# Kernel tuning notes

Measured on AMD Instinct MI355X. Metric: run time of the kernel, lower is better.

Reference implementation:

```python
import jax, jax.numpy as jnp
import numpy as np

B, N, C, DP, H, P = 1, 768, 384, 128, 12, 4
HP3 = H * P * 3


def setup_inputs() -> dict:
    key = jax.random.key(0)
    ks = jax.random.split(key, 16)
    w = lambda k, shp: (jax.random.normal(k, shp, jnp.float32) * 0.02)
    inp = {
        'single': jax.random.normal(ks[0], (B, N, C), jnp.float32),
        'pair': jax.random.normal(ks[1], (B, N, N, DP), jnp.float32),
        'rot': jax.random.normal(ks[2], (B, N, 3, 3), jnp.float32),
        'trans': jax.random.normal(ks[3], (B, N, 3), jnp.float32),
        'q_w': w(ks[4], (C, C)), 'q_b': jnp.zeros((C,), jnp.float32),
        'k_w': w(ks[5], (C, C)), 'k_b': jnp.zeros((C,), jnp.float32),
        'v_w': w(ks[6], (C, C)), 'v_b': jnp.zeros((C,), jnp.float32),
        'pb_w': w(ks[7], (H, DP)), 'pb_b': jnp.zeros((H,), jnp.float32),
        'qp_w': w(ks[8], (HP3, C)), 'qp_b': jnp.zeros((HP3,), jnp.float32),
        'kp_w': w(ks[9], (HP3, C)), 'kp_b': jnp.zeros((HP3,), jnp.float32),
        'vp_w': w(ks[10], (HP3, C)), 'vp_b': jnp.zeros((HP3,), jnp.float32),
        'pt_w': w(ks[11], (C, HP3)), 'pt_b': jnp.zeros((C,), jnp.float32),
        'out_w': w(ks[12], (C, C)), 'out_b': jnp.zeros((C,), jnp.float32),
        'ln_g': jnp.ones((C,), jnp.float32), 'ln_b': jnp.zeros((C,), jnp.float32),
    }
    return inp


def _lin(x, w, b):
    return x @ w.T + b


def reference(single, pair, rot, trans, q_w, q_b, k_w, k_b, v_w, v_b,
              pb_w, pb_b, qp_w, qp_b, kp_w, kp_b, vp_w, vp_b,
              pt_w, pt_b, out_w, out_b, ln_g, ln_b):
    Bs, Ns, Cs = single.shape
    Ch = Cs // H
    scale = Ch ** (-0.5)

    q = _lin(single, q_w, q_b).reshape(Bs, Ns, H, Ch)
    k = _lin(single, k_w, k_b).reshape(Bs, Ns, H, Ch)
    v = _lin(single, v_w, v_b).reshape(Bs, Ns, H, Ch)

    pair_bias = jnp.transpose(_lin(pair, pb_w, pb_b), (0, 3, 1, 2))  # b h i j

    def to_global(w_, b_):
        pts = _lin(single, w_, b_).reshape(Bs, Ns, H, P, 3)
        return jnp.einsum('bnhpi,bnij->bnhpj', pts, rot) + trans[:, :, None, None, :]

    qg = to_global(qp_w, qp_b)
    kg = to_global(kp_w, kp_b)

    q2 = jnp.sum(qg * qg, axis=(3, 4))  # b n h
    k2 = jnp.sum(kg * kg, axis=(3, 4))
    qk = jnp.einsum('bihpd,bjhpd->bijh', qg, kg)
    point_logits = -0.5 * (q2[:, :, None, :] + k2[:, None, :, :] - 2.0 * qk)  # b i j h
    point_logits = jnp.transpose(point_logits, (0, 3, 1, 2)) * scale  # b h i j

    scalar_logits = jnp.einsum('bnhc,bmhc->bhnm', q, k) * scale
    attn = jax.nn.softmax(scalar_logits + pair_bias + point_logits, axis=-1)

    weighted = jnp.einsum('bhnm,bmhc->bnhc', attn, v).reshape(Bs, Ns, Cs)

    vg = to_global(vp_w, vp_b)
    point_weighted = jnp.einsum('bhnm,bmhpd->bnhpd', attn, vg).reshape(Bs, Ns, HP3)
    point_proj = _lin(point_weighted, pt_w, pt_b)

    out = _lin(weighted + point_proj, out_w, out_b)
    x = single + out
    mu = jnp.mean(x, axis=-1, keepdims=True)
    var = jnp.var(x, axis=-1, keepdims=True)
    return (x - mu) / jnp.sqrt(var + 1e-5) * ln_g + ln_b
```

## Files before the change

kernel.cpp:

```cpp
#include <hip/hip_runtime.h>
#include <hip/hip_bf16.h>
#include <cstddef>

#define NN 768
#define CC 384
#define HH 12
#define DPP 128
#define OFF_Q   0
#define OFF_K   294912
#define OFF_V   589824
#define OFF_QP  884736
#define OFF_KP  995328
#define OFF_VP  1105920
#define OFF_WTD 1216512
#define OFF_PW  1511424
#define OFF_LOG 1622016

__global__ __launch_bounds__(256) void k_proj(
    const float* __restrict__ single,
    const float* __restrict__ qw, const float* __restrict__ qb,
    const float* __restrict__ kw, const float* __restrict__ kb,
    const float* __restrict__ vw, const float* __restrict__ vb,
    const float* __restrict__ qpw, const float* __restrict__ qpb,
    const float* __restrict__ kpw, const float* __restrict__ kpb,
    const float* __restrict__ vpw, const float* __restrict__ vpb,
    float* __restrict__ ws)
{
    __shared__ float As[64][33];
    __shared__ float Bs[48][33];
    const int tid = threadIdx.x;
    const int i0 = blockIdx.y * 64;
    const int n0 = blockIdx.x * 48;
    const int tx = tid & 15, ty = tid >> 4;
    float acc[4][3] = {};
    for (int k0 = 0; k0 < CC; k0 += 32) {
        #pragma unroll
        for (int l = tid; l < 64 * 32; l += 256) {
            int r = l >> 5, c = l & 31;
            As[r][c] = single[(size_t)(i0 + r) * CC + k0 + c];
        }
        #pragma unroll
        for (int l = tid; l < 48 * 32; l += 256) {
            int r = l >> 5, c = l & 31;
            int n = n0 + r;
            const float* wp; int row;
            if (n < 1152) { int m = n / CC; row = n - m * CC; wp = (m == 0) ? qw : ((m == 1) ? kw : vw); }
            else { int np = n - 1152; int m = np / 144; row = np - m * 144; wp = (m == 0) ? qpw : ((m == 1) ? kpw : vpw); }
            Bs[r][c] = wp[(size_t)row * CC + k0 + c];
        }
        __syncthreads();
        #pragma unroll
        for (int kk = 0; kk < 32; ++kk) {
            float av[4], bv[3];
            #pragma unroll
            for (int a = 0; a < 4; ++a) av[a] = As[ty * 4 + a][kk];
            #pragma unroll
            for (int b = 0; b < 3; ++b) bv[b] = Bs[tx * 3 + b][kk];
            #pragma unroll
            for (int a = 0; a < 4; ++a)
                #pragma unroll
                for (int b = 0; b < 3; ++b)
                    acc[a][b] = fmaf(av[a], bv[b], acc[a][b]);
        }
        __syncthreads();
    }
    #pragma unroll
    for (int a = 0; a < 4; ++a) {
        int i = i0 + ty * 4 + a;
        #pragma unroll
        for (int b = 0; b < 3; ++b) {
            int n = n0 + tx * 3 + b;
            float bias; size_t dst;
            if (n < 1152) {
                int m = n / CC; int c = n - m * CC;
                bias = ((m == 0) ? qb : ((m == 1) ? kb : vb))[c];
                dst = (size_t)m * 294912 + (size_t)i * CC + c;
            } else {
                int np = n - 1152; int m = np / 144; int c = np - m * 144;
                bias = ((m == 0) ? qpb : ((m == 1) ? kpb : vpb))[c];
                dst = (size_t)OFF_QP + (size_t)m * 110592 + (size_t)i * 144 + c;
            }
            ws[dst] = acc[a][b] + bias;
        }
    }
}

__global__ __launch_bounds__(256) void k_to_global(
    const float* __restrict__ rot, const float* __restrict__ trans, float* __restrict__ ws)
{
    int id = blockIdx.x * 256 + threadIdx.x;
    if (id >= 3 * NN * 48) return;
    int t3 = id / (NN * 48);
    int rem = id - t3 * (NN * 48);
    int n = rem / 48;
    int hp = rem - n * 48;
    float* arr = ws + OFF_QP + (size_t)t3 * 110592 + (size_t)n * 144 + hp * 3;
    float p0 = arr[0], p1 = arr[1], p2 = arr[2];
    const float* R = rot + (size_t)n * 9;
    const float* T = trans + (size_t)n * 3;
    arr[0] = p0 * R[0] + p1 * R[3] + p2 * R[6] + T[0];
    arr[1] = p0 * R[1] + p1 * R[4] + p2 * R[7] + T[1];
    arr[2] = p0 * R[2] + p1 * R[5] + p2 * R[8] + T[2];
}

__global__ __launch_bounds__(256) void k_logits(
    const float* __restrict__ pair,
    const float* __restrict__ pbw, const float* __restrict__ pbb,
    const float* __restrict__ q, const float* __restrict__ k,
    const float* __restrict__ qg, const float* __restrict__ kg,
    float* __restrict__ logits)
{
    const float scale = 0.17677669529663687f;
    __shared__ float pbw_s[HH * DPP];
    const int tid = threadIdx.x;
    for (int idx = tid; idx < HH * DPP; idx += 256) pbw_s[idx] = pbw[idx];
    __syncthreads();
    const int i0 = blockIdx.x * 4;
    const int j = blockIdx.y * 256 + tid;

    float acc[4][12];
    #pragma unroll
    for (int ii = 0; ii < 4; ++ii)
        #pragma unroll
        for (int h = 0; h < HH; ++h) acc[ii][h] = pbb[h];

    #pragma unroll
    for (int ii = 0; ii < 4; ++ii) {
        const float4* pr = (const float4*)(pair + ((size_t)(i0 + ii) * NN + j) * DPP);
        #pragma unroll 4
        for (int k4 = 0; k4 < 32; ++k4) {
            float4 pv = pr[k4];
            #pragma unroll
            for (int h = 0; h < HH; ++h) {
                float4 w = ((const float4*)pbw_s)[h * 32 + k4];
                acc[ii][h] = fmaf(pv.x, w.x, acc[ii][h]);
                acc[ii][h] = fmaf(pv.y, w.y, acc[ii][h]);
                acc[ii][h] = fmaf(pv.z, w.z, acc[ii][h]);
                acc[ii][h] = fmaf(pv.w, w.w, acc[ii][h]);
            }
        }
    }

    #pragma unroll
    for (int h = 0; h < HH; ++h) {
        float kf[32];
        const float4* kp4 = (const float4*)(k + (size_t)j * CC + h * 32);
        #pragma unroll
        for (int t = 0; t < 8; ++t) {
            float4 tv = kp4[t];
            kf[4 * t + 0] = tv.x; kf[4 * t + 1] = tv.y; kf[4 * t + 2] = tv.z; kf[4 * t + 3] = tv.w;
        }
        float kgf[12];
        const float4* kg4 = (const float4*)(kg + (size_t)j * 144 + h * 12);
        #pragma unroll
        for (int t = 0; t < 3; ++t) {
            float4 tv = kg4[t];
            kgf[4 * t + 0] = tv.x; kgf[4 * t + 1] = tv.y; kgf[4 * t + 2] = tv.z; kgf[4 * t + 3] = tv.w;
        }
        #pragma unroll
        for (int ii = 0; ii < 4; ++ii) {
            const float* qrow = q + (size_t)(i0 + ii) * CC + h * 32;
            float dt = 0.f;
            #pragma unroll
            for (int c = 0; c < 32; ++c) dt = fmaf(kf[c], qrow[c], dt);
            const float* qgrow = qg + (size_t)(i0 + ii) * 144 + h * 12;
            float pt = 0.f;
            #pragma unroll
            for (int e = 0; e < 12; ++e) { float d2 = qgrow[e] - kgf[e]; pt = fmaf(d2, d2, pt); }
            float lv = acc[ii][h] + scale * dt - 0.5f * scale * pt;
            logits[((size_t)h * NN + (i0 + ii)) * NN + j] = lv;
        }
    }
}

__global__ __launch_bounds__(256) void k_soft(
    const float* __restrict__ logits, const float* __restrict__ v, const float* __restrict__ vg,
    float* __restrict__ weighted, float* __restrict__ pw)
{
    __shared__ float att[8][772];
    __shared__ float vt[128][45];
    const int tid = threadIdx.x;
    const int h = blockIdx.y;
    const int i0 = blockIdx.x * 8;

    for (int idx = tid; idx < 8 * 192; idx += 256) {
        int r = idx / 192, c4 = idx - r * 192;
        float4 tv = ((const float4*)(logits + ((size_t)h * NN + i0 + r) * NN))[c4];
        float* dp = &att[r][c4 * 4];
        dp[0] = tv.x; dp[1] = tv.y; dp[2] = tv.z; dp[3] = tv.w;
    }
    __syncthreads();
    {
        int r = tid >> 5, lane = tid & 31;
        float m = -1e30f;
        for (int jj = lane; jj < NN; jj += 32) m = fmaxf(m, att[r][jj]);
        #pragma unroll
        for (int off = 16; off; off >>= 1) m = fmaxf(m, __shfl_xor(m, off, 32));
        float s = 0.f;
        for (int jj = lane; jj < NN; jj += 32) { float e = __expf(att[r][jj] - m); att[r][jj] = e; s += e; }
        #pragma unroll
        for (int off = 16; off; off >>= 1) s += __shfl_xor(s, off, 32);
        float inv = 1.f / s;
        for (int jj = lane; jj < NN; jj += 32) att[r][jj] *= inv;
    }
    __syncthreads();

    float acc0 = 0.f, acc1 = 0.f;
    const int o0 = tid, o1 = tid + 256;
    const int r0 = o0 / 44, d0 = o0 - r0 * 44;
    const int o1c = (o1 < 352) ? o1 : 351;
    const int r1 = o1c / 44, d1 = o1c - r1 * 44;
    for (int jc = 0; jc < 6; ++jc) {
        for (int idx = tid; idx < 128 * 44; idx += 256) {
            int jj = idx / 44, d = idx - jj * 44;
            int jg = jc * 128 + jj;
            vt[jj][d] = (d < 32) ? v[(size_t)jg * CC + h * 32 + d]
                                 : vg[(size_t)jg * 144 + h * 12 + (d - 32)];
        }
        __syncthreads();
        const float* a0p = &att[r0][jc * 128];
        const float* a1p = &att[r1][jc * 128];
        #pragma unroll 4
        for (int jj = 0; jj < 128; ++jj) {
            acc0 = fmaf(a0p[jj], vt[jj][d0], acc0);
            acc1 = fmaf(a1p[jj], vt[jj][d1], acc1);
        }
        __syncthreads();
    }
    {
        int i = i0 + r0;
        if (d0 < 32) weighted[(size_t)i * CC + h * 32 + d0] = acc0;
        else         pw[(size_t)i * 144 + h * 12 + (d0 - 32)] = acc0;
    }
    if (o1 < 352) {
        int i = i0 + r1;
        if (d1 < 32) weighted[(size_t)i * CC + h * 32 + d1] = acc1;
        else         pw[(size_t)i * 144 + h * 12 + (d1 - 32)] = acc1;
    }
}

__global__ __launch_bounds__(384) void k_out(
    const float* __restrict__ single,
    const float* __restrict__ weighted, const float* __restrict__ pwv,
    const float* __restrict__ ptw, const float* __restrict__ ptb,
    const float* __restrict__ outw, const float* __restrict__ outb,
    const float* __restrict__ lng, const float* __restrict__ lnb,
    float* __restrict__ out)
{
    __shared__ float pw_s[4][144];
    __shared__ float tmp_s[4][388];
    __shared__ float red[16];
    const int tid = threadIdx.x;
    const int i0 = blockIdx.x * 4;
    for (int idx = tid; idx < 4 * 144; idx += 384) {
        int r = idx / 144, e = idx - r * 144;
        pw_s[r][e] = pwv[(size_t)(i0 + r) * 144 + e];
    }
    __syncthreads();
    const int c = tid;
    float t[4];
    {
        float a[4] = {0.f, 0.f, 0.f, 0.f};
        const float4* wp4 = (const float4*)(ptw + (size_t)c * 144);
        #pragma unroll 4
        for (int e4 = 0; e4 < 36; ++e4) {
            float4 w4 = wp4[e4];
            #pragma unroll
            for (int r = 0; r < 4; ++r) {
                float4 pv = *(const float4*)&pw_s[r][e4 * 4];
                a[r] = fmaf(w4.x, pv.x, a[r]);
                a[r] = fmaf(w4.y, pv.y, a[r]);
                a[r] = fmaf(w4.z, pv.z, a[r]);
                a[r] = fmaf(w4.w, pv.w, a[r]);
            }
        }
        float pb = ptb[c];
        #pragma unroll
        for (int r = 0; r < 4; ++r)
            t[r] = weighted[(size_t)(i0 + r) * CC + c] + pb + a[r];
    }
    #pragma unroll
    for (int r = 0; r < 4; ++r) tmp_s[r][c] = t[r];
    __syncthreads();
    float o[4];
    {
        float ob = outb[c];
        #pragma unroll
        for (int r = 0; r < 4; ++r) o[r] = ob;
        const float4* wp4 = (const float4*)(outw + (size_t)c * CC);
        #pragma unroll 2
        for (int e4 = 0; e4 < 96; ++e4) {
            float4 w4 = wp4[e4];
            #pragma unroll
            for (int r = 0; r < 4; ++r) {
                float4 tv = *(const float4*)&tmp_s[r][e4 * 4];
                o[r] = fmaf(w4.x, tv.x, o[r]);
                o[r] = fmaf(w4.y, tv.y, o[r]);
                o[r] = fmaf(w4.z, tv.z, o[r]);
                o[r] = fmaf(w4.w, tv.w, o[r]);
            }
        }
        #pragma unroll
        for (int r = 0; r < 4; ++r) o[r] += single[(size_t)(i0 + r) * CC + c];
    }
    float g = lng[c], bb = lnb[c];
    #pragma unroll
    for (int rr = 0; rr < 4; ++rr) {
        float xs = o[rr], xq = o[rr] * o[rr];
        #pragma unroll
        for (int off = 32; off; off >>= 1) {
            xs += __shfl_xor(xs, off, 64);
            xq += __shfl_xor(xq, off, 64);
        }
        __syncthreads();
        if ((tid & 63) == 0) { int w = tid >> 6; red[w] = xs; red[8 + w] = xq; }
        __syncthreads();
        float S = red[0] + red[1] + red[2] + red[3] + red[4] + red[5];
        float Q = red[8] + red[9] + red[10] + red[11] + red[12] + red[13];
        float mu = S * (1.f / 384.f);
        float var = Q * (1.f / 384.f) - mu * mu;
        float rs = rsqrtf(var + 1e-5f);
        out[(size_t)(i0 + rr) * CC + c] = (o[rr] - mu) * rs * g + bb;
    }
}

extern "C" void kernel_launch(void* const* d_in, const int* in_sizes, int n_in,
                              void* d_out, int out_size, void* d_ws, size_t ws_size,
                              hipStream_t stream)
{
    const float* single = (const float*)d_in[0];
    const float* pair   = (const float*)d_in[1];
    const float* rot    = (const float*)d_in[2];
    const float* trans  = (const float*)d_in[3];
    const float* qw  = (const float*)d_in[4];  const float* qb  = (const float*)d_in[5];
    const float* kw  = (const float*)d_in[6];  const float* kb  = (const float*)d_in[7];
    const float* vw  = (const float*)d_in[8];  const float* vb  = (const float*)d_in[9];
    const float* pbw = (const float*)d_in[10]; const float* pbb = (const float*)d_in[11];
    const float* qpw = (const float*)d_in[12]; const float* qpb = (const float*)d_in[13];
    const float* kpw = (const float*)d_in[14]; const float* kpb = (const float*)d_in[15];
    const float* vpw = (const float*)d_in[16]; const float* vpb = (const float*)d_in[17];
    const float* ptw = (const float*)d_in[18]; const float* ptb = (const float*)d_in[19];
    const float* outw = (const float*)d_in[20]; const float* outb = (const float*)d_in[21];
    const float* lng  = (const float*)d_in[22]; const float* lnb  = (const float*)d_in[23];

    float* ws = (float*)d_ws;
    float* q   = ws + OFF_Q;
    float* k   = ws + OFF_K;
    float* v   = ws + OFF_V;
    float* qg  = ws + OFF_QP;
    float* kg  = ws + OFF_KP;
    float* vg  = ws + OFF_VP;
    float* wtd = ws + OFF_WTD;
    float* pwv = ws + OFF_PW;
    float* logits = ws + OFF_LOG;

    dim3 g1(33, 12);
    hipLaunchKernelGGL(k_proj, g1, dim3(256), 0, stream,
                       single, qw, qb, kw, kb, vw, vb, qpw, qpb, kpw, kpb, vpw, vpb, ws);
    hipLaunchKernelGGL(k_to_global, dim3(432), dim3(256), 0, stream, rot, trans, ws);
    dim3 g3(192, 3);
    hipLaunchKernelGGL(k_logits, g3, dim3(256), 0, stream,
                       pair, pbw, pbb, q, k, qg, kg, logits);
    dim3 g4(96, 12);
    hipLaunchKernelGGL(k_soft, g4, dim3(256), 0, stream, logits, v, vg, wtd, pwv);
    hipLaunchKernelGGL(k_out, dim3(192), dim3(384), 0, stream,
                       single, wtd, pwv, ptw, ptb, outw, outb, lng, lnb, (float*)d_out);
}
```

Before: 320.7 us.

## Transpose V/VG storage, read directly in softmax-AV, halve logits rows per block

The projection kernel now writes V and the value points transposed (feature-major, sequence contiguous), and a new kernel rotates those points in that layout. The softmax kernel drops its shared-memory staging of V and has 176 threads stream float4 rows of V straight from global memory against the attention rows. The logits kernel now handles 2 query rows per block instead of 4 (twice as many blocks) and reads pair-bias weights directly from global memory instead of shared memory. The goal is fewer syncs and shared-memory traffic plus more parallelism, at the cost of idle threads in the softmax kernel and more global or cached weight reads.

```diff
diff --git a/kernel.cpp b/kernel.cpp
--- a/kernel.cpp
+++ b/kernel.cpp
@@ -74,11 +74,13 @@
             if (n < 1152) {
                 int m = n / CC; int c = n - m * CC;
                 bias = ((m == 0) ? qb : ((m == 1) ? kb : vb))[c];
-                dst = (size_t)m * 294912 + (size_t)i * CC + c;
+                if (m == 2) dst = (size_t)OFF_V + (size_t)c * NN + i;
+                else        dst = (size_t)m * 294912 + (size_t)i * CC + c;
             } else {
                 int np = n - 1152; int m = np / 144; int c = np - m * 144;
                 bias = ((m == 0) ? qpb : ((m == 1) ? kpb : vpb))[c];
-                dst = (size_t)OFF_QP + (size_t)m * 110592 + (size_t)i * 144 + c;
+                if (m == 2) dst = (size_t)OFF_VP + (size_t)c * NN + i;
+                else        dst = (size_t)OFF_QP + (size_t)m * 110592 + (size_t)i * 144 + c;
             }
             ws[dst] = acc[a][b] + bias;
         }
@@ -89,7 +91,7 @@
     const float* __restrict__ rot, const float* __restrict__ trans, float* __restrict__ ws)
 {
     int id = blockIdx.x * 256 + threadIdx.x;
-    if (id >= 3 * NN * 48) return;
+    if (id >= 2 * NN * 48) return;
     int t3 = id / (NN * 48);
     int rem = id - t3 * (NN * 48);
     int n = rem / 48;
@@ -103,6 +105,24 @@
     arr[2] = p0 * R[2] + p1 * R[5] + p2 * R[8] + T[2];
 }
 
+__global__ __launch_bounds__(256) void k_to_global_v(
+    const float* __restrict__ rot, const float* __restrict__ trans, float* __restrict__ ws)
+{
+    int id = blockIdx.x * 256 + threadIdx.x;
+    if (id >= 48 * NN) return;
+    int hp = id / NN;
+    int n = id - hp * NN;
+    float* r0 = ws + OFF_VP + (size_t)(hp * 3 + 0) * NN + n;
+    float* r1 = ws + OFF_VP + (size_t)(hp * 3 + 1) * NN + n;
+    float* r2 = ws + OFF_VP + (size_t)(hp * 3 + 2) * NN + n;
+    float p0 = *r0, p1 = *r1, p2 = *r2;
+    const float* R = rot + (size_t)n * 9;
+    const float* T = trans + (size_t)n * 3;
+    *r0 = p0 * R[0] + p1 * R[3] + p2 * R[6] + T[0];
+    *r1 = p0 * R[1] + p1 * R[4] + p2 * R[7] + T[1];
+    *r2 = p0 * R[2] + p1 * R[5] + p2 * R[8] + T[2];
+}
+
 __global__ __launch_bounds__(256) void k_logits(
     const float* __restrict__ pair,
     const float* __restrict__ pbw, const float* __restrict__ pbb,
@@ -111,33 +131,35 @@
     float* __restrict__ logits)
 {
     const float scale = 0.17677669529663687f;
-    __shared__ float pbw_s[HH * DPP];
     const int tid = threadIdx.x;
-    for (int idx = tid; idx < HH * DPP; idx += 256) pbw_s[idx] = pbw[idx];
-    __syncthreads();
-    const int i0 = blockIdx.x * 4;
+    const int i0 = blockIdx.x * 2;
     const int j = blockIdx.y * 256 + tid;
 
-    float acc[4][12];
-    #pragma unroll
-    for (int ii = 0; ii < 4; ++ii)
+    float acc[2][12];
+    #pragma unroll
+    for (int ii = 0; ii < 2; ++ii)
         #pragma unroll
         for (int h = 0; h < HH; ++h) acc[ii][h] = pbb[h];
 
-    #pragma unroll
-    for (int ii = 0; ii < 4; ++ii) {
-        const float4* pr = (const float4*)(pair + ((size_t)(i0 + ii) * NN + j) * DPP);
-        #pragma unroll 4
-        for (int k4 = 0; k4 < 32; ++k4) {
-            float4 pv = pr[k4];
-            #pragma unroll
-            for (int h = 0; h < HH; ++h) {
-                float4 w = ((const float4*)pbw_s)[h * 32 + k4];
-                acc[ii][h] = fmaf(pv.x, w.x, acc[ii][h]);
-                acc[ii][h] = fmaf(pv.y, w.y, acc[ii][h]);
-                acc[ii][h] = fmaf(pv.z, w.z, acc[ii][h]);
-                acc[ii][h] = fmaf(pv.w, w.w, acc[ii][h]);
-            }
+    const float4* pr0 = (const float4*)(pair + ((size_t)(i0 + 0) * NN + j) * DPP);
+    const float4* pr1 = (const float4*)(pair + ((size_t)(i0 + 1) * NN + j) * DPP);
+    const float4* w4 = (const float4*)pbw;
+
+    #pragma unroll 4
+    for (int k4 = 0; k4 < 32; ++k4) {
+        float4 p0 = pr0[k4];
+        float4 p1 = pr1[k4];
+        #pragma unroll
+        for (int h = 0; h < HH; ++h) {
+            float4 w = w4[h * 32 + k4];
+            acc[0][h] = fmaf(p0.x, w.x, acc[0][h]);
+            acc[0][h] = fmaf(p0.y, w.y, acc[0][h]);
+            acc[0][h] = fmaf(p0.z, w.z, acc[0][h]);
+            acc[0][h] = fmaf(p0.w, w.w, acc[0][h]);
+            acc[1][h] = fmaf(p1.x, w.x, acc[1][h]);
+            acc[1][h] = fmaf(p1.y, w.y, acc[1][h]);
+            acc[1][h] = fmaf(p1.z, w.z, acc[1][h]);
+            acc[1][h] = fmaf(p1.w, w.w, acc[1][h]);
         }
     }
 
@@ -158,7 +180,7 @@
             kgf[4 * t + 0] = tv.x; kgf[4 * t + 1] = tv.y; kgf[4 * t + 2] = tv.z; kgf[4 * t + 3] = tv.w;
         }
         #pragma unroll
-        for (int ii = 0; ii < 4; ++ii) {
+        for (int ii = 0; ii < 2; ++ii) {
             const float* qrow = q + (size_t)(i0 + ii) * CC + h * 32;
             float dt = 0.f;
             #pragma unroll
@@ -174,11 +196,10 @@
 }
 
 __global__ __launch_bounds__(256) void k_soft(
-    const float* __restrict__ logits, const float* __restrict__ v, const float* __restrict__ vg,
+    const float* __restrict__ logits, const float* __restrict__ ws_base,
     float* __restrict__ weighted, float* __restrict__ pw)
 {
-    __shared__ float att[8][772];
-    __shared__ float vt[128][45];
+    __shared__ float att[8][776];
     const int tid = threadIdx.x;
     const int h = blockIdx.y;
     const int i0 = blockIdx.x * 8;
@@ -205,35 +226,30 @@
     }
     __syncthreads();
 
-    float acc0 = 0.f, acc1 = 0.f;
-    const int o0 = tid, o1 = tid + 256;
-    const int r0 = o0 / 44, d0 = o0 - r0 * 44;
-    const int o1c = (o1 < 352) ? o1 : 351;
-    const int r1 = o1c / 44, d1 = o1c - r1 * 44;
-    for (int jc = 0; jc < 6; ++jc) {
-        for (int idx = tid; idx < 128 * 44; idx += 256) {
-            int jj = idx / 44, d = idx - jj * 44;
-            int jg = jc * 128 + jj;
-            vt[jj][d] = (d < 32) ? v[(size_t)jg * CC + h * 32 + d]
-                                 : vg[(size_t)jg * 144 + h * 12 + (d - 32)];
-        }
-        __syncthreads();
-        const float* a0p = &att[r0][jc * 128];
-        const float* a1p = &att[r1][jc * 128];
+    if (tid < 176) {
+        const int r = tid / 22, dp2 = tid - r * 22;
+        const int d0 = 2 * dp2, d1 = d0 + 1;
+        const float* row0 = (d0 < 32) ? (ws_base + OFF_V  + (size_t)(h * 32 + d0) * NN)
+                                      : (ws_base + OFF_VP + (size_t)(h * 12 + (d0 - 32)) * NN);
+        const float* row1 = (d1 < 32) ? (ws_base + OFF_V  + (size_t)(h * 32 + d1) * NN)
+                                      : (ws_base + OFF_VP + (size_t)(h * 12 + (d1 - 32)) * NN);
+        const float4* x0 = (const float4*)row0;
+        const float4* x1 = (const float4*)row1;
+        const float4* a4 = (const float4*)&att[r][0];
+        float acc0 = 0.f, acc1 = 0.f;
         #pragma unroll 4
-        for (int jj = 0; jj < 128; ++jj) {
-            acc0 = fmaf(a0p[jj], vt[jj][d0], acc0);
-            acc1 = fmaf(a1p[jj], vt[jj][d1], acc1);
-        }
-        __syncthreads();
-    }
-    {
-        int i = i0 + r0;
+        for (int j4 = 0; j4 < 192; ++j4) {
+            float4 a = a4[j4];
+            float4 b0 = x0[j4];
+            float4 b1 = x1[j4];
+            acc0 = fmaf(a.x, b0.x, acc0); acc0 = fmaf(a.y, b0.y, acc0);
+            acc0 = fmaf(a.z, b0.z, acc0); acc0 = fmaf(a.w, b0.w, acc0);
+            acc1 = fmaf(a.x, b1.x, acc1); acc1 = fmaf(a.y, b1.y, acc1);
+            acc1 = fmaf(a.z, b1.z, acc1); acc1 = fmaf(a.w, b1.w, acc1);
+        }
+        int i = i0 + r;
         if (d0 < 32) weighted[(size_t)i * CC + h * 32 + d0] = acc0;
         else         pw[(size_t)i * 144 + h * 12 + (d0 - 32)] = acc0;
-    }
-    if (o1 < 352) {
-        int i = i0 + r1;
         if (d1 < 32) weighted[(size_t)i * CC + h * 32 + d1] = acc1;
         else         pw[(size_t)i * 144 + h * 12 + (d1 - 32)] = acc1;
     }
@@ -346,10 +362,8 @@
     float* ws = (float*)d_ws;
     float* q   = ws + OFF_Q;
     float* k   = ws + OFF_K;
-    float* v   = ws + OFF_V;
     float* qg  = ws + OFF_QP;
     float* kg  = ws + OFF_KP;
-    float* vg  = ws + OFF_VP;
     float* wtd = ws + OFF_WTD;
     float* pwv = ws + OFF_PW;
     float* logits = ws + OFF_LOG;
@@ -357,12 +371,13 @@
     dim3 g1(33, 12);
     hipLaunchKernelGGL(k_proj, g1, dim3(256), 0, stream,
                        single, qw, qb, kw, kb, vw, vb, qpw, qpb, kpw, kpb, vpw, vpb, ws);
-    hipLaunchKernelGGL(k_to_global, dim3(432), dim3(256), 0, stream, rot, trans, ws);
-    dim3 g3(192, 3);
+    hipLaunchKernelGGL(k_to_global, dim3(288), dim3(256), 0, stream, rot, trans, ws);
+    hipLaunchKernelGGL(k_to_global_v, dim3(144), dim3(256), 0, stream, rot, trans, ws);
+    dim3 g3(384, 3);
     hipLaunchKernelGGL(k_logits, g3, dim3(256), 0, stream,
                        pair, pbw, pbb, q, k, qg, kg, logits);
     dim3 g4(96, 12);
-    hipLaunchKernelGGL(k_soft, g4, dim3(256), 0, stream, logits, v, vg, wtd, pwv);
+    hipLaunchKernelGGL(k_soft, g4, dim3(256), 0, stream, logits, ws, wtd, pwv);
     hipLaunchKernelGGL(k_out, dim3(192), dim3(384), 0, stream,
                        single, wtd, pwv, ptw, ptb, outw, outb, lng, lnb, (float*)d_out);
 }
```

New measurement: 466.9 us. 45.6% more time.

## Split logits kernel into pair-bias projection and scalar/point attention kernels

Applied to the files above, without the earlier changes.

The fused logits kernel is split in two. k_pairbias computes the pair-bias projection, one row i per block, reading pbw straight from global memory instead of staging it in LDS. k_qk runs on a 3D grid over (i-chunk, j-chunk, head) and reuses each thread's k and kg registers across 48 query rows, then does a read-modify-write to add its terms into the logits. This gives more parallelism and lower register pressure per kernel, at the cost of an extra launch and a second full read and write of the 28 MB logits buffer.

```diff
diff --git a/kernel.cpp b/kernel.cpp
--- a/kernel.cpp
+++ b/kernel.cpp
@@ -103,73 +103,80 @@
     arr[2] = p0 * R[2] + p1 * R[5] + p2 * R[8] + T[2];
 }
 
-__global__ __launch_bounds__(256) void k_logits(
+__global__ __launch_bounds__(256) void k_pairbias(
     const float* __restrict__ pair,
     const float* __restrict__ pbw, const float* __restrict__ pbb,
+    float* __restrict__ logits)
+{
+    const int tid = threadIdx.x;
+    const int i = blockIdx.x;
+    const int j = blockIdx.y * 256 + tid;
+
+    float acc[12];
+    #pragma unroll
+    for (int h = 0; h < HH; ++h) acc[h] = pbb[h];
+
+    const float4* pr = (const float4*)(pair + ((size_t)i * NN + j) * DPP);
+    const float4* w4 = (const float4*)pbw;
+
+    #pragma unroll 4
+    for (int k4 = 0; k4 < 32; ++k4) {
+        float4 p = pr[k4];
+        #pragma unroll
+        for (int h = 0; h < HH; ++h) {
+            float4 w = w4[h * 32 + k4];
+            acc[h] = fmaf(p.x, w.x, acc[h]);
+            acc[h] = fmaf(p.y, w.y, acc[h]);
+            acc[h] = fmaf(p.z, w.z, acc[h]);
+            acc[h] = fmaf(p.w, w.w, acc[h]);
+        }
+    }
+    #pragma unroll
+    for (int h = 0; h < HH; ++h)
+        logits[((size_t)h * NN + i) * NN + j] = acc[h];
+}
+
+__global__ __launch_bounds__(256) void k_qk(
     const float* __restrict__ q, const float* __restrict__ k,
     const float* __restrict__ qg, const float* __restrict__ kg,
     float* __restrict__ logits)
 {
     const float scale = 0.17677669529663687f;
-    __shared__ float pbw_s[HH * DPP];
-    const int tid = threadIdx.x;
-    for (int idx = tid; idx < HH * DPP; idx += 256) pbw_s[idx] = pbw[idx];
-    __syncthreads();
-    const int i0 = blockIdx.x * 4;
-    const int j = blockIdx.y * 256 + tid;
-
-    float acc[4][12];
-    #pragma unroll
-    for (int ii = 0; ii < 4; ++ii)
-        #pragma unroll
-        for (int h = 0; h < HH; ++h) acc[ii][h] = pbb[h];
-
-    #pragma unroll
-    for (int ii = 0; ii < 4; ++ii) {
-        const float4* pr = (const float4*)(pair + ((size_t)(i0 + ii) * NN + j) * DPP);
-        #pragma unroll 4
-        for (int k4 = 0; k4 < 32; ++k4) {
-            float4 pv = pr[k4];
-            #pragma unroll
-            for (int h = 0; h < HH; ++h) {
-                float4 w = ((const float4*)pbw_s)[h * 32 + k4];
-                acc[ii][h] = fmaf(pv.x, w.x, acc[ii][h]);
-                acc[ii][h] = fmaf(pv.y, w.y, acc[ii][h]);
-                acc[ii][h] = fmaf(pv.z, w.z, acc[ii][h]);
-                acc[ii][h] = fmaf(pv.w, w.w, acc[ii][h]);
-            }
-        }
-    }
-
-    #pragma unroll
-    for (int h = 0; h < HH; ++h) {
-        float kf[32];
-        const float4* kp4 = (const float4*)(k + (size_t)j * CC + h * 32);
-        #pragma unroll
-        for (int t = 0; t < 8; ++t) {
-            float4 tv = kp4[t];
-            kf[4 * t + 0] = tv.x; kf[4 * t + 1] = tv.y; kf[4 * t + 2] = tv.z; kf[4 * t + 3] = tv.w;
-        }
-        float kgf[12];
-        const float4* kg4 = (const float4*)(kg + (size_t)j * 144 + h * 12);
-        #pragma unroll
-        for (int t = 0; t < 3; ++t) {
-            float4 tv = kg4[t];
-            kgf[4 * t + 0] = tv.x; kgf[4 * t + 1] = tv.y; kgf[4 * t + 2] = tv.z; kgf[4 * t + 3] = tv.w;
-        }
-        #pragma unroll
-        for (int ii = 0; ii < 4; ++ii) {
-            const float* qrow = q + (size_t)(i0 + ii) * CC + h * 32;
-            float dt = 0.f;
-            #pragma unroll
-            for (int c = 0; c < 32; ++c) dt = fmaf(kf[c], qrow[c], dt);
-            const float* qgrow = qg + (size_t)(i0 + ii) * 144 + h * 12;
-            float pt = 0.f;
-            #pragma unroll
-            for (int e = 0; e < 12; ++e) { float d2 = qgrow[e] - kgf[e]; pt = fmaf(d2, d2, pt); }
-            float lv = acc[ii][h] + scale * dt - 0.5f * scale * pt;
-            logits[((size_t)h * NN + (i0 + ii)) * NN + j] = lv;
-        }
+    const int tid = threadIdx.x;
+    const int i0 = blockIdx.x * 48;
+    const int jc = blockIdx.y;
+    const int h  = blockIdx.z;
+    const int j  = jc * 256 + tid;
+
+    float kf[32];
+    const float4* kp4 = (const float4*)(k + (size_t)j * CC + h * 32);
+    #pragma unroll
+    for (int t = 0; t < 8; ++t) {
+        float4 tv = kp4[t];
+        kf[4 * t + 0] = tv.x; kf[4 * t + 1] = tv.y; kf[4 * t + 2] = tv.z; kf[4 * t + 3] = tv.w;
+    }
+    float kgf[12];
+    const float4* kg4 = (const float4*)(kg + (size_t)j * 144 + h * 12);
+    #pragma unroll
+    for (int t = 0; t < 3; ++t) {
+        float4 tv = kg4[t];
+        kgf[4 * t + 0] = tv.x; kgf[4 * t + 1] = tv.y; kgf[4 * t + 2] = tv.z; kgf[4 * t + 3] = tv.w;
+    }
+
+    #pragma unroll 4
+    for (int ii = 0; ii < 48; ++ii) {
+        const int i = i0 + ii;
+        size_t idx = ((size_t)h * NN + i) * NN + j;
+        float old = logits[idx];
+        const float* qrow = q + (size_t)i * CC + h * 32;
+        float dt = 0.f;
+        #pragma unroll
+        for (int c = 0; c < 32; ++c) dt = fmaf(kf[c], qrow[c], dt);
+        const float* qgrow = qg + (size_t)i * 144 + h * 12;
+        float pt = 0.f;
+        #pragma unroll
+        for (int e = 0; e < 12; ++e) { float d2 = qgrow[e] - kgf[e]; pt = fmaf(d2, d2, pt); }
+        logits[idx] = old + scale * dt - 0.5f * scale * pt;
     }
 }
 
@@ -358,9 +365,10 @@
     hipLaunchKernelGGL(k_proj, g1, dim3(256), 0, stream,
                        single, qw, qb, kw, kb, vw, vb, qpw, qpb, kpw, kpb, vpw, vpb, ws);
     hipLaunchKernelGGL(k_to_global, dim3(432), dim3(256), 0, stream, rot, trans, ws);
-    dim3 g3(192, 3);
-    hipLaunchKernelGGL(k_logits, g3, dim3(256), 0, stream,
-                       pair, pbw, pbb, q, k, qg, kg, logits);
+    dim3 g3a(768, 3);
+    hipLaunchKernelGGL(k_pairbias, g3a, dim3(256), 0, stream, pair, pbw, pbb, logits);
+    dim3 g3b(16, 3, 12);
+    hipLaunchKernelGGL(k_qk, g3b, dim3(256), 0, stream, q, k, qg, kg, logits);
     dim3 g4(96, 12);
     hipLaunchKernelGGL(k_soft, g4, dim3(256), 0, stream, logits, v, vg, wtd, pwv);
     hipLaunchKernelGGL(k_out, dim3(192), dim3(384), 0, stream,
```

After: 378.3 us. 18.0% more time.

## Split pair-bias into coalesced kernel and fuse scalar/point logits into softmax

Applied to the files above, without the earlier changes.

The logits kernel is split. A new pair-bias kernel stages pair rows through shared memory with register prefetch, so global loads are coalesced instead of each thread striding 512 bytes per row. The scalar and point logit terms move into the softmax kernel, which tiles k/kg into shared memory and adds them to the pair bias already in shared memory. The intent is to cut the uncoalesced pair traffic, which dominates the 302 MB read. The cost is extra per-block staging and loop passes in the softmax kernel, and q rows are read repeatedly from global memory there.

```diff
diff --git a/kernel.cpp b/kernel.cpp
--- a/kernel.cpp
+++ b/kernel.cpp
@@ -103,82 +103,75 @@
     arr[2] = p0 * R[2] + p1 * R[5] + p2 * R[8] + T[2];
 }
 
-__global__ __launch_bounds__(256) void k_logits(
+__global__ __launch_bounds__(256) void k_pairbias(
     const float* __restrict__ pair,
     const float* __restrict__ pbw, const float* __restrict__ pbb,
+    float* __restrict__ logits)
+{
+    __shared__ float sp[256][33];
+    const int tid = threadIdx.x;
+    const int i = blockIdx.x;
+    const int j0 = blockIdx.y * 256;
+    const float4* w4 = (const float4*)pbw;
+
+    float acc[12];
+    #pragma unroll
+    for (int h = 0; h < HH; ++h) acc[h] = pbb[h];
+
+    const int lrow = tid >> 3;
+    const int lcol = tid & 7;
+    const float* pbase = pair + ((size_t)i * NN + j0) * DPP;
+
+    float4 st[8];
+    #pragma unroll
+    for (int p = 0; p < 8; ++p) {
+        int row = p * 32 + lrow;
+        st[p] = *(const float4*)(pbase + (size_t)row * DPP + lcol * 4);
+    }
+
+    for (int cc = 0; cc < 4; ++cc) {
+        #pragma unroll
+        for (int p = 0; p < 8; ++p) {
+            int row = p * 32 + lrow;
+            *(float4*)&sp[row][lcol * 4] = st[p];
+        }
+        __syncthreads();
+        if (cc < 3) {
+            #pragma unroll
+            for (int p = 0; p < 8; ++p) {
+                int row = p * 32 + lrow;
+                st[p] = *(const float4*)(pbase + (size_t)row * DPP + (cc + 1) * 32 + lcol * 4);
+            }
+        }
+        #pragma unroll
+        for (int c4 = 0; c4 < 8; ++c4) {
+            float4 pv = *(const float4*)&sp[tid][c4 * 4];
+            #pragma unroll
+            for (int h = 0; h < HH; ++h) {
+                float4 w = w4[h * 32 + cc * 8 + c4];
+                acc[h] = fmaf(pv.x, w.x, acc[h]);
+                acc[h] = fmaf(pv.y, w.y, acc[h]);
+                acc[h] = fmaf(pv.z, w.z, acc[h]);
+                acc[h] = fmaf(pv.w, w.w, acc[h]);
+            }
+        }
+        __syncthreads();
+    }
+    #pragma unroll
+    for (int h = 0; h < HH; ++h)
+        logits[((size_t)h * NN + i) * NN + j0 + tid] = acc[h];
+}
+
+__global__ __launch_bounds__(256) void k_soft(
+    const float* __restrict__ logits,
     const float* __restrict__ q, const float* __restrict__ k,
     const float* __restrict__ qg, const float* __restrict__ kg,
-    float* __restrict__ logits)
+    const float* __restrict__ v, const float* __restrict__ vg,
+    float* __restrict__ weighted, float* __restrict__ pw)
 {
     const float scale = 0.17677669529663687f;
-    __shared__ float pbw_s[HH * DPP];
-    const int tid = threadIdx.x;
-    for (int idx = tid; idx < HH * DPP; idx += 256) pbw_s[idx] = pbw[idx];
-    __syncthreads();
-    const int i0 = blockIdx.x * 4;
-    const int j = blockIdx.y * 256 + tid;
-
-    float acc[4][12];
-    #pragma unroll
-    for (int ii = 0; ii < 4; ++ii)
-        #pragma unroll
-        for (int h = 0; h < HH; ++h) acc[ii][h] = pbb[h];
-
-    #pragma unroll
-    for (int ii = 0; ii < 4; ++ii) {
-        const float4* pr = (const float4*)(pair + ((size_t)(i0 + ii) * NN + j) * DPP);
-        #pragma unroll 4
-        for (int k4 = 0; k4 < 32; ++k4) {
-            float4 pv = pr[k4];
-            #pragma unroll
-            for (int h = 0; h < HH; ++h) {
-                float4 w = ((const float4*)pbw_s)[h * 32 + k4];
-                acc[ii][h] = fmaf(pv.x, w.x, acc[ii][h]);
-                acc[ii][h] = fmaf(pv.y, w.y, acc[ii][h]);
-                acc[ii][h] = fmaf(pv.z, w.z, acc[ii][h]);
-                acc[ii][h] = fmaf(pv.w, w.w, acc[ii][h]);
-            }
-        }
-    }
-
-    #pragma unroll
-    for (int h = 0; h < HH; ++h) {
-        float kf[32];
-        const float4* kp4 = (const float4*)(k + (size_t)j * CC + h * 32);
-        #pragma unroll
-        for (int t = 0; t < 8; ++t) {
-            float4 tv = kp4[t];
-            kf[4 * t + 0] = tv.x; kf[4 * t + 1] = tv.y; kf[4 * t + 2] = tv.z; kf[4 * t + 3] = tv.w;
-        }
-        float kgf[12];
-        const float4* kg4 = (const float4*)(kg + (size_t)j * 144 + h * 12);
-        #pragma unroll
-        for (int t = 0; t < 3; ++t) {
-            float4 tv = kg4[t];
-            kgf[4 * t + 0] = tv.x; kgf[4 * t + 1] = tv.y; kgf[4 * t + 2] = tv.z; kgf[4 * t + 3] = tv.w;
-        }
-        #pragma unroll
-        for (int ii = 0; ii < 4; ++ii) {
-            const float* qrow = q + (size_t)(i0 + ii) * CC + h * 32;
-            float dt = 0.f;
-            #pragma unroll
-            for (int c = 0; c < 32; ++c) dt = fmaf(kf[c], qrow[c], dt);
-            const float* qgrow = qg + (size_t)(i0 + ii) * 144 + h * 12;
-            float pt = 0.f;
-            #pragma unroll
-            for (int e = 0; e < 12; ++e) { float d2 = qgrow[e] - kgf[e]; pt = fmaf(d2, d2, pt); }
-            float lv = acc[ii][h] + scale * dt - 0.5f * scale * pt;
-            logits[((size_t)h * NN + (i0 + ii)) * NN + j] = lv;
-        }
-    }
-}
-
-__global__ __launch_bounds__(256) void k_soft(
-    const float* __restrict__ logits, const float* __restrict__ v, const float* __restrict__ vg,
-    float* __restrict__ weighted, float* __restrict__ pw)
-{
     __shared__ float att[8][772];
-    __shared__ float vt[128][45];
+    __shared__ float st[128][44];
     const int tid = threadIdx.x;
     const int h = blockIdx.y;
     const int i0 = blockIdx.x * 8;
@@ -190,6 +183,45 @@
         dp[0] = tv.x; dp[1] = tv.y; dp[2] = tv.z; dp[3] = tv.w;
     }
     __syncthreads();
+
+    for (int jc = 0; jc < 6; ++jc) {
+        for (int idx = tid; idx < 128 * 44; idx += 256) {
+            int jj = idx / 44, d = idx - jj * 44;
+            int jg = jc * 128 + jj;
+            st[jj][d] = (d < 32) ? k[(size_t)jg * CC + h * 32 + d]
+                                 : kg[(size_t)jg * 144 + h * 12 + (d - 32)];
+        }
+        __syncthreads();
+        #pragma unroll
+        for (int pass = 0; pass < 4; ++pass) {
+            int idx2 = pass * 256 + tid;
+            int r = idx2 >> 7, jj = idx2 & 127;
+            const float* qrow  = q  + (size_t)(i0 + r) * CC + h * 32;
+            const float* qgrow = qg + (size_t)(i0 + r) * 144 + h * 12;
+            const float4* kt4 = (const float4*)&st[jj][0];
+            float kf[32];
+            #pragma unroll
+            for (int t = 0; t < 8; ++t) {
+                float4 tv = kt4[t];
+                kf[4*t+0] = tv.x; kf[4*t+1] = tv.y; kf[4*t+2] = tv.z; kf[4*t+3] = tv.w;
+            }
+            float kgf[12];
+            #pragma unroll
+            for (int t = 0; t < 3; ++t) {
+                float4 tv = kt4[8 + t];
+                kgf[4*t+0] = tv.x; kgf[4*t+1] = tv.y; kgf[4*t+2] = tv.z; kgf[4*t+3] = tv.w;
+            }
+            float dt = 0.f;
+            #pragma unroll
+            for (int c = 0; c < 32; ++c) dt = fmaf(kf[c], qrow[c], dt);
+            float pt = 0.f;
+            #pragma unroll
+            for (int e = 0; e < 12; ++e) { float d2 = qgrow[e] - kgf[e]; pt = fmaf(d2, d2, pt); }
+            att[r][jc * 128 + jj] += scale * dt - 0.5f * scale * pt;
+        }
+        __syncthreads();
+    }
+
     {
         int r = tid >> 5, lane = tid & 31;
         float m = -1e30f;
@@ -214,7 +246,7 @@
         for (int idx = tid; idx < 128 * 44; idx += 256) {
             int jj = idx / 44, d = idx - jj * 44;
             int jg = jc * 128 + jj;
-            vt[jj][d] = (d < 32) ? v[(size_t)jg * CC + h * 32 + d]
+            st[jj][d] = (d < 32) ? v[(size_t)jg * CC + h * 32 + d]
                                  : vg[(size_t)jg * 144 + h * 12 + (d - 32)];
         }
         __syncthreads();
@@ -222,8 +254,8 @@
         const float* a1p = &att[r1][jc * 128];
         #pragma unroll 4
         for (int jj = 0; jj < 128; ++jj) {
-            acc0 = fmaf(a0p[jj], vt[jj][d0], acc0);
-            acc1 = fmaf(a1p[jj], vt[jj][d1], acc1);
+            acc0 = fmaf(a0p[jj], st[jj][d0], acc0);
+            acc1 = fmaf(a1p[jj], st[jj][d1], acc1);
         }
         __syncthreads();
     }
@@ -358,11 +390,11 @@
     hipLaunchKernelGGL(k_proj, g1, dim3(256), 0, stream,
                        single, qw, qb, kw, kb, vw, vb, qpw, qpb, kpw, kpb, vpw, vpb, ws);
     hipLaunchKernelGGL(k_to_global, dim3(432), dim3(256), 0, stream, rot, trans, ws);
-    dim3 g3(192, 3);
-    hipLaunchKernelGGL(k_logits, g3, dim3(256), 0, stream,
-                       pair, pbw, pbb, q, k, qg, kg, logits);
+    dim3 g3(768, 3);
+    hipLaunchKernelGGL(k_pairbias, g3, dim3(256), 0, stream, pair, pbw, pbb, logits);
     dim3 g4(96, 12);
-    hipLaunchKernelGGL(k_soft, g4, dim3(256), 0, stream, logits, v, vg, wtd, pwv);
+    hipLaunchKernelGGL(k_soft, g4, dim3(256), 0, stream,
+                       logits, q, k, qg, kg, v, vg, wtd, pwv);
     hipLaunchKernelGGL(k_out, dim3(192), dim3(384), 0, stream,
                        single, wtd, pwv, ptw, ptb, outw, outb, lng, lnb, (float*)d_out);
 }
```

Result: slower. 616.1 us (+92.1%).
